# Optimization experiments

Measured on AMD Instinct MI355X. Metric: run time of the kernel, lower is better.

## Reference

```python
import jax, jax.numpy as jnp
import numpy as np

S = 4096   # decoder sequence length
T = 4096   # encoder sequence length
D = 2048   # x_size == qk_size (required for q @ k^T to typecheck)


def setup_inputs() -> dict:
    key = jax.random.key(0)
    k1, k2, k3, k4 = jax.random.split(key, 4)
    x_vectors = jax.random.normal(k1, (S, D), dtype=jnp.float32)
    enc_output = jax.random.normal(k2, (2, T, S), dtype=jnp.float32) * 0.02
    Wq = jax.random.normal(k3, (D, D), dtype=jnp.float32) * 0.02
    bq = jax.random.normal(k4, (D,), dtype=jnp.float32) * 0.02
    return {"x_vectors": x_vectors, "enc_output": enc_output, "Wq": Wq, "bq": bq}


def reference(x_vectors, enc_output, Wq, bq):
    # q = Linear(x): [S, D]
    q = x_vectors @ Wq.T + bq
    # k, v produced by matmul of encoder-output matrices with x: [T, D]
    k = enc_output[0] @ x_vectors
    v = enc_output[1] @ x_vectors
    # attention scores [S, T], scaled by sqrt(qk_size)
    e = (q @ k.T) / jnp.sqrt(jnp.float32(D))
    # softmax over dim=1 (last axis of the rank-2 score matrix)
    a = jax.nn.softmax(e, axis=1)
    # z = a @ v^T: [S, D]
    z = a @ v
    return z
```

## Files before the change

kernel.cpp:

```cpp
#include <hip/hip_runtime.h>


typedef __attribute__((ext_vector_type(8))) __bf16 bf16x8;
typedef __attribute__((ext_vector_type(4))) float f32x4;
typedef __attribute__((ext_vector_type(4))) unsigned short ushort4v;
typedef __attribute__((ext_vector_type(8))) unsigned short ushort8v;

#define S_DIM 4096
#define T_DIM 4096
#define D_DIM 2048

__device__ __forceinline__ unsigned short f2bf(float f) {
    unsigned int u = __float_as_uint(f);
    u += 0x7fffu + ((u >> 16) & 1u);
    return (unsigned short)(u >> 16);
}

__device__ __forceinline__ void block_sync() {
    __builtin_amdgcn_sched_barrier(0);
    __builtin_amdgcn_s_barrier();
    __builtin_amdgcn_sched_barrier(0);
}

#define GL(gptr, sptr)                                                        \
    __builtin_amdgcn_global_load_lds(                                         \
        (__attribute__((address_space(1))) void*)(void*)(gptr),               \
        (__attribute__((address_space(3))) void*)(sptr), 16, 0, 0)

__device__ __forceinline__ f32x4 MFMA(bf16x8 a, bf16x8 b, f32x4 c) {
    return __builtin_amdgcn_mfma_f32_16x16x32_bf16(a, b, c, 0, 0, 0);
}

__global__ __launch_bounds__(256)
void k_convert(const float* __restrict__ in, unsigned short* __restrict__ out, long n) {
    long i = ((long)blockIdx.x * blockDim.x + threadIdx.x) * 8;
    const long stride = (long)gridDim.x * blockDim.x * 8;
    for (; i < n; i += stride) {
        float4 a = *(const float4*)(in + i);
        float4 b = *(const float4*)(in + i + 4);
        ushort8v o;
        o[0] = f2bf(a.x); o[1] = f2bf(a.y); o[2] = f2bf(a.z); o[3] = f2bf(a.w);
        o[4] = f2bf(b.x); o[5] = f2bf(b.y); o[6] = f2bf(b.z); o[7] = f2bf(b.w);
        *(ushort8v*)(out + i) = o;
    }
}

__global__ __launch_bounds__(256)
void k_transpose(const float* __restrict__ in, unsigned short* __restrict__ out,
                 int R, int C) {
    __shared__ float tile[32][33];
    const int bx = blockIdx.x * 32;
    const int by = blockIdx.y * 32;
    const int tx = threadIdx.x;
    const int ty = threadIdx.y;
    #pragma unroll
    for (int i = 0; i < 32; i += 8)
        tile[ty + i][tx] = in[(long)(by + ty + i) * C + bx + tx];
    __syncthreads();
    #pragma unroll
    for (int i = 0; i < 32; i += 8)
        out[(long)(bx + ty + i) * R + by + tx] = f2bf(tile[tx][ty + i]);
}

__global__ __launch_bounds__(256)
void k_transpose_bf(const unsigned short* __restrict__ in,
                    unsigned short* __restrict__ out, int R, int C) {
    __shared__ unsigned short tile[32][33];
    const int bx = blockIdx.x * 32;
    const int by = blockIdx.y * 32;
    const int tx = threadIdx.x;
    const int ty = threadIdx.y;
    #pragma unroll
    for (int i = 0; i < 32; i += 8)
        tile[ty + i][tx] = in[(long)(by + ty + i) * C + bx + tx];
    __syncthreads();
    #pragma unroll
    for (int i = 0; i < 32; i += 8)
        out[(long)(bx + ty + i) * R + by + tx] = tile[tx][ty + i];
}

template<bool STG, bool PF, int VMW>
__device__ __forceinline__ void seg8(
    const unsigned short* (&gA)[2], const int (&ldA)[2],
    const unsigned short* (&gB)[2], const int (&ldB)[2],
    const char* cur, const char* nxt, char* stg, int arB, int brB,
    bf16x8 (&Ac)[8], bf16x8 (&B01c)[2], bf16x8 (&B23)[2],
    bf16x8 (&An)[8], bf16x8 (&B01n)[2],
    f32x4 (&acc)[8][4])
{
    B23[0] = *(const bf16x8*)(cur + brB + 2048);
    B23[1] = *(const bf16x8*)(cur + brB + 3072);
    if constexpr (STG) {
        GL(gA[0], stg + ldA[0]); gA[0] += 32;
        GL(gA[1], stg + ldA[1]); gA[1] += 32;
    }
    block_sync();
    asm volatile("s_waitcnt lgkmcnt(2)" ::: "memory");
    __builtin_amdgcn_sched_barrier(0);
    __builtin_amdgcn_s_setprio(1);
    #pragma unroll
    for (int m = 0; m < 8; ++m) {
        acc[m][0] = MFMA(Ac[m], B01c[0], acc[m][0]);
        acc[m][1] = MFMA(Ac[m], B01c[1], acc[m][1]);
    }
    __builtin_amdgcn_s_setprio(0);
    if constexpr (PF) {
        #pragma unroll
        for (int m = 0; m < 8; ++m)
            An[m] = *(const bf16x8*)(nxt + arB + m * 1024);
        B01n[0] = *(const bf16x8*)(nxt + brB);
        B01n[1] = *(const bf16x8*)(nxt + brB + 1024);
    }
    if constexpr (STG) {
        GL(gB[0], stg + ldB[0]); gB[0] += 32;
        GL(gB[1], stg + ldB[1]); gB[1] += 32;
    }
    if constexpr (VMW == 4)      asm volatile("s_waitcnt vmcnt(4)" ::: "memory");
    else if constexpr (VMW == 0) asm volatile("s_waitcnt vmcnt(0)" ::: "memory");
    block_sync();
    if constexpr (PF) asm volatile("s_waitcnt lgkmcnt(10)" ::: "memory");
    else              asm volatile("s_waitcnt lgkmcnt(0)" ::: "memory");
    __builtin_amdgcn_sched_barrier(0);
    __builtin_amdgcn_s_setprio(1);
    #pragma unroll
    for (int m = 0; m < 8; ++m) {
        acc[m][2] = MFMA(Ac[m], B23[0], acc[m][2]);
        acc[m][3] = MFMA(Ac[m], B23[1], acc[m][3]);
    }
    __builtin_amdgcn_s_setprio(0);
}

template<bool STG, bool PF, int VMW>
__device__ __forceinline__ void seg4(
    const unsigned short* (&gA)[2], const int (&ldA)[2],
    const unsigned short* (&gB)[2], const int (&ldB)[2],
    const char* nxt, char* stg, int arB, int brB,
    bf16x8 (&Ac)[4], bf16x8 (&Bc)[4],
    bf16x8 (&An)[4], bf16x8 (&Bn)[4],
    f32x4 (&acc)[4][4])
{
    if constexpr (PF) {
        #pragma unroll
        for (int m = 0; m < 4; ++m)
            An[m] = *(const bf16x8*)(nxt + arB + m * 1024);
        #pragma unroll
        for (int n = 0; n < 4; ++n)
            Bn[n] = *(const bf16x8*)(nxt + brB + n * 1024);
    }
    if constexpr (STG) {
        GL(gA[0], stg + ldA[0]); gA[0] += 32;
        GL(gB[0], stg + ldB[0]); gB[0] += 32;
        GL(gB[1], stg + ldB[1]); gB[1] += 32;
    }
    if constexpr (VMW == 3)      asm volatile("s_waitcnt vmcnt(3)" ::: "memory");
    else if constexpr (VMW == 0) asm volatile("s_waitcnt vmcnt(0)" ::: "memory");
    block_sync();
    if constexpr (PF) asm volatile("s_waitcnt lgkmcnt(8)" ::: "memory");
    else              asm volatile("s_waitcnt lgkmcnt(0)" ::: "memory");
    __builtin_amdgcn_sched_barrier(0);
    __builtin_amdgcn_s_setprio(1);
    #pragma unroll
    for (int m = 0; m < 4; ++m)
        #pragma unroll
        for (int n = 0; n < 4; ++n)
            acc[m][n] = MFMA(Ac[m], Bc[n], acc[m][n]);
    __builtin_amdgcn_s_setprio(0);
}

template<int MFR, int OUT_BF16, int HAS_BIAS>
__global__ __launch_bounds__(512, 2)
void k_gemm(const unsigned short* __restrict__ A,
            const unsigned short* __restrict__ B,
            const float* __restrict__ bias,
            void* __restrict__ C,
            int M, int N, int K, float alpha) {
    constexpr int BM   = MFR * 32;
    constexpr int LPTA = (BM * 4) / 512;
    constexpr int LDSA = BM * 64;
    constexpr int SLOT = LDSA + 16384;
    extern __shared__ __align__(16) char smem[];

    const int tid = threadIdx.x;
    const int l = tid & 63;
    const int w = tid >> 6;
    const int wr = w >> 2;
    const int wc = w & 3;

    const int gx = gridDim.x, gy = gridDim.y;
    const int flat = blockIdx.y * gx + blockIdx.x;
    const int per = (gx * gy) >> 3;
    const int wid = (flat & 7) * per + (flat >> 3);
    const int sc = wid / (gy * 4);
    const int rm = wid - sc * gy * 4;
    const int by = rm >> 2;
    const int bx = sc * 4 + (rm & 3);

    const long brow = (long)by * BM;
    const long bcol = (long)bx * 256;
    const int NT = K >> 5;

    const unsigned short* gA[2];
    int ldA[2];
    #pragma unroll
    for (int j = 0; j < LPTA; ++j) {
        const int q = (w * LPTA + j) * 64 + l;
        const int R = q >> 2;
        const int c = (q & 3) ^ ((R >> 1) & 3);
        gA[j] = A + (brow + R) * (long)K + c * 8;
        ldA[j] = q * 16;
    }
    const unsigned short* gB[2];
    int ldB[2];
    #pragma unroll
    for (int j = 0; j < 2; ++j) {
        const int q = (w * 2 + j) * 64 + l;
        const int R = q >> 2;
        const int c = (q & 3) ^ ((R >> 1) & 3);
        gB[j] = B + (bcol + R) * (long)K + c * 8;
        ldB[j] = LDSA + q * 16;
    }

    const int sAB = (((l >> 4) ^ ((l >> 1) & 3)) << 4);
    const int arB = (wr * (MFR * 16) + (l & 15)) * 64 + sAB;
    const int brB = LDSA + (wc * 64 + (l & 15)) * 64 + sAB;

    char* const b0 = smem;
    char* const b1 = smem + SLOT;
    char* const b2 = smem + 2 * SLOT;
    char* const b3 = smem + 3 * SLOT;

    f32x4 acc[MFR][4] = {};

    {
        char* d = smem;
        #pragma unroll
        for (int tt = 0; tt < 3; ++tt) {
            #pragma unroll
            for (int j = 0; j < LPTA; ++j) { GL(gA[j], d + ldA[j]); gA[j] += 32; }
            #pragma unroll
            for (int j = 0; j < 2; ++j)    { GL(gB[j], d + ldB[j]); gB[j] += 32; }
            d += SLOT;
        }
        if constexpr (MFR == 8) asm volatile("s_waitcnt vmcnt(4)" ::: "memory");
        else                    asm volatile("s_waitcnt vmcnt(3)" ::: "memory");
        block_sync();
    }

    if constexpr (MFR == 8) {
        bf16x8 Aa[8], Ab[8], Ba[2], Bb[2], B23[2];
        #pragma unroll
        for (int m = 0; m < 8; ++m) Aa[m] = *(const bf16x8*)(b0 + arB + m * 1024);
        Ba[0] = *(const bf16x8*)(b0 + brB);
        Ba[1] = *(const bf16x8*)(b0 + brB + 1024);

        for (int t = 0; t + 8 <= NT; t += 4) {
            seg8<true, true, 4>(gA, ldA, gB, ldB, b0, b1, b3, arB, brB,
                                Aa, Ba, B23, Ab, Bb, acc);
            seg8<true, true, 4>(gA, ldA, gB, ldB, b1, b2, b0, arB, brB,
                                Ab, Bb, B23, Aa, Ba, acc);
            seg8<true, true, 4>(gA, ldA, gB, ldB, b2, b3, b1, arB, brB,
                                Aa, Ba, B23, Ab, Bb, acc);
            seg8<true, true, 4>(gA, ldA, gB, ldB, b3, b0, b2, arB, brB,
                                Ab, Bb, B23, Aa, Ba, acc);
        }
        seg8<true,  true,  4>(gA, ldA, gB, ldB, b0, b1, b3, arB, brB,
                              Aa, Ba, B23, Ab, Bb, acc);
        seg8<false, true,  0>(gA, ldA, gB, ldB, b1, b2, b3, arB, brB,
                              Ab, Bb, B23, Aa, Ba, acc);
        seg8<false, true, -1>(gA, ldA, gB, ldB, b2, b3, b3, arB, brB,
                              Aa, Ba, B23, Ab, Bb, acc);
        seg8<false, false, -1>(gA, ldA, gB, ldB, b3, b0, b3, arB, brB,
                               Ab, Bb, B23, Aa, Ba, acc);
    } else {
        bf16x8 Aa[4], Ab[4], Ba[4], Bb[4];
        #pragma unroll
        for (int m = 0; m < 4; ++m) Aa[m] = *(const bf16x8*)(b0 + arB + m * 1024);
        #pragma unroll
        for (int n = 0; n < 4; ++n) Ba[n] = *(const bf16x8*)(b0 + brB + n * 1024);

        for (int t = 0; t + 8 <= NT; t += 4) {
            seg4<true, true, 3>(gA, ldA, gB, ldB, b1, b3, arB, brB, Aa, Ba, Ab, Bb, acc);
            seg4<true, true, 3>(gA, ldA, gB, ldB, b2, b0, arB, brB, Ab, Bb, Aa, Ba, acc);
            seg4<true, true, 3>(gA, ldA, gB, ldB, b3, b1, arB, brB, Aa, Ba, Ab, Bb, acc);
            seg4<true, true, 3>(gA, ldA, gB, ldB, b0, b2, arB, brB, Ab, Bb, Aa, Ba, acc);
        }
        seg4<true,  true,  3>(gA, ldA, gB, ldB, b1, b3, arB, brB, Aa, Ba, Ab, Bb, acc);
        seg4<false, true,  0>(gA, ldA, gB, ldB, b2, b3, arB, brB, Ab, Bb, Aa, Ba, acc);
        seg4<false, true, -1>(gA, ldA, gB, ldB, b3, b3, arB, brB, Aa, Ba, Ab, Bb, acc);
        seg4<false, false, -1>(gA, ldA, gB, ldB, b3, b3, arB, brB, Ab, Bb, Aa, Ba, acc);
    }

    const long crow0 = brow + wr * (MFR * 16) + (l >> 4) * 4;
    const long ccol0 = bcol + wc * 64 + (l & 15);
    #pragma unroll
    for (int n = 0; n < 4; ++n) {
        const long col = ccol0 + n * 16;
        const float bb = HAS_BIAS ? bias[col] : 0.0f;
        #pragma unroll
        for (int m = 0; m < MFR; ++m) {
            #pragma unroll
            for (int r = 0; r < 4; ++r) {
                const long row = crow0 + m * 16 + r;
                const float v = acc[m][n][r] * alpha + bb;
                if (OUT_BF16)
                    ((unsigned short*)C)[row * N + col] = f2bf(v);
                else
                    ((float*)C)[row * N + col] = v;
            }
        }
    }
}

__global__ __launch_bounds__(256)
void k_softmax(const float* __restrict__ E, unsigned short* __restrict__ A, int T) {
    const long row = blockIdx.x;
    const float* er = E + row * (long)T;
    const int t = threadIdx.x;
    const int l = t & 63;
    const int w = t >> 6;

    float4 v[4];
    float m = -3.4e38f;
    #pragma unroll
    for (int j = 0; j < 4; ++j) {
        v[j] = *(const float4*)(er + j * 1024 + t * 4);
        m = fmaxf(m, fmaxf(fmaxf(v[j].x, v[j].y), fmaxf(v[j].z, v[j].w)));
    }
    #pragma unroll
    for (int o = 32; o > 0; o >>= 1) m = fmaxf(m, __shfl_xor(m, o));

    __shared__ float redm[4];
    __shared__ float reds[4];
    if (l == 0) redm[w] = m;
    __syncthreads();
    m = fmaxf(fmaxf(redm[0], redm[1]), fmaxf(redm[2], redm[3]));

    float s = 0.f;
    #pragma unroll
    for (int j = 0; j < 4; ++j) {
        v[j].x = __expf(v[j].x - m); s += v[j].x;
        v[j].y = __expf(v[j].y - m); s += v[j].y;
        v[j].z = __expf(v[j].z - m); s += v[j].z;
        v[j].w = __expf(v[j].w - m); s += v[j].w;
    }
    #pragma unroll
    for (int o = 32; o > 0; o >>= 1) s += __shfl_xor(s, o);
    if (l == 0) reds[w] = s;
    __syncthreads();
    s = reds[0] + reds[1] + reds[2] + reds[3];
    const float inv = 1.0f / s;

    unsigned short* ar = A + row * (long)T;
    #pragma unroll
    for (int j = 0; j < 4; ++j) {
        ushort4v o4;
        o4[0] = f2bf(v[j].x * inv);
        o4[1] = f2bf(v[j].y * inv);
        o4[2] = f2bf(v[j].z * inv);
        o4[3] = f2bf(v[j].w * inv);
        *(ushort4v*)(ar + j * 1024 + t * 4) = o4;
    }
}

extern "C" void kernel_launch(void* const* d_in, const int* in_sizes, int n_in,
                              void* d_out, int out_size, void* d_ws, size_t ws_size,
                              hipStream_t stream) {
    const float* x   = (const float*)d_in[0];
    const float* enc = (const float*)d_in[1];
    const float* Wq  = (const float*)d_in[2];
    const float* bq  = (const float*)d_in[3];
    float* out = (float*)d_out;
    char* ws = (char*)d_ws;

    unsigned short* abf   = (unsigned short*)(ws);
    unsigned short* xT    = (unsigned short*)(ws);
    unsigned short* xbf   = (unsigned short*)(ws + (16L << 20));
    unsigned short* wqbf  = (unsigned short*)(ws + (32L << 20));
    unsigned short* qbf   = (unsigned short*)(ws + (40L << 20));
    unsigned short* kv    = (unsigned short*)(ws + (56L << 20));
    unsigned short* vT    = (unsigned short*)(ws + (88L << 20));
    unsigned short* encbf = (unsigned short*)(ws + (104L << 20));
    float*          e     = (float*)(ws + (104L << 20));

    k_convert<<<4096, 256, 0, stream>>>(x,   xbf,   (long)S_DIM * D_DIM);
    k_convert<<<4096, 256, 0, stream>>>(Wq,  wqbf,  (long)D_DIM * D_DIM);
    k_convert<<<4096, 256, 0, stream>>>(enc, encbf, 2L * T_DIM * S_DIM);
    k_transpose<<<dim3(D_DIM / 32, S_DIM / 32), dim3(32, 8), 0, stream>>>(x, xT, S_DIM, D_DIM);

    #define LAUNCH_G(MFRV, OB, HB, Ap, Bp, biasp, Cp, M_, N_, K_, al)                      \
        do {                                                                               \
            constexpr int smemB = (MFRV * 32 * 64 + 16384) * 4;                            \
            hipFuncSetAttribute((const void*)k_gemm<MFRV, OB, HB>,                         \
                                hipFuncAttributeMaxDynamicSharedMemorySize, smemB);        \
            k_gemm<MFRV, OB, HB><<<dim3((N_) / 256, (M_) / (MFRV * 32)), 512, smemB,       \
                                   stream>>>(Ap, Bp, biasp, Cp, M_, N_, K_, al);           \
        } while (0)

    LAUNCH_G(4, 1, 1, xbf, wqbf, bq, qbf, S_DIM, D_DIM, D_DIM, 1.0f);
    LAUNCH_G(8, 1, 0, encbf, xT, nullptr, kv, 2 * T_DIM, D_DIM, S_DIM, 1.0f);
    k_transpose_bf<<<dim3(D_DIM / 32, T_DIM / 32), dim3(32, 8), 0, stream>>>(
        kv + (long)T_DIM * D_DIM, vT, T_DIM, D_DIM);
    LAUNCH_G(8, 0, 0, qbf, kv, nullptr, e, S_DIM, T_DIM, D_DIM, 0.022097086912079608f);
    k_softmax<<<S_DIM, 256, 0, stream>>>(e, abf, T_DIM);
    LAUNCH_G(4, 0, 0, abf, vT, nullptr, out, S_DIM, D_DIM, T_DIM, 1.0f);
}
```

Before: 377.1 us.

## Use 32x32x16 MFMA in large-tile GEMM and fuse x conversion into transpose

The MFR=8 GEMM path switches from 16x16x32 to 32x32x16 bf16 MFMA instructions, reworking LDS read addressing (XOR-swizzled halves), accumulator layout and the epilogue row mapping. Larger MFMA tiles cut instruction count and fragment reuse overhead. Separately, the x-to-bf16 conversion kernel is merged into the transpose kernel, which now writes both layouts from one read of x. The risk is higher register pressure and a less coalesced epilogue store pattern.

```diff
diff --git a/kernel.cpp b/kernel.cpp
--- a/kernel.cpp
+++ b/kernel.cpp
@@ -3,6 +3,7 @@
 
 typedef __attribute__((ext_vector_type(8))) __bf16 bf16x8;
 typedef __attribute__((ext_vector_type(4))) float f32x4;
+typedef __attribute__((ext_vector_type(16))) float f32x16;
 typedef __attribute__((ext_vector_type(4))) unsigned short ushort4v;
 typedef __attribute__((ext_vector_type(8))) unsigned short ushort8v;
 
@@ -27,8 +28,11 @@
         (__attribute__((address_space(1))) void*)(void*)(gptr),               \
         (__attribute__((address_space(3))) void*)(sptr), 16, 0, 0)
 
-__device__ __forceinline__ f32x4 MFMA(bf16x8 a, bf16x8 b, f32x4 c) {
+__device__ __forceinline__ f32x4 MFMA16(bf16x8 a, bf16x8 b, f32x4 c) {
     return __builtin_amdgcn_mfma_f32_16x16x32_bf16(a, b, c, 0, 0, 0);
+}
+__device__ __forceinline__ f32x16 MFMA32(bf16x8 a, bf16x8 b, f32x16 c) {
+    return __builtin_amdgcn_mfma_f32_32x32x16_bf16(a, b, c, 0, 0, 0);
 }
 
 __global__ __launch_bounds__(256)
@@ -46,20 +50,24 @@
 }
 
 __global__ __launch_bounds__(256)
-void k_transpose(const float* __restrict__ in, unsigned short* __restrict__ out,
-                 int R, int C) {
+void k_transpose_dual(const float* __restrict__ in,
+                      unsigned short* __restrict__ outT,
+                      unsigned short* __restrict__ outN, int R, int C) {
     __shared__ float tile[32][33];
     const int bx = blockIdx.x * 32;
     const int by = blockIdx.y * 32;
     const int tx = threadIdx.x;
     const int ty = threadIdx.y;
     #pragma unroll
+    for (int i = 0; i < 32; i += 8) {
+        float v = in[(long)(by + ty + i) * C + bx + tx];
+        tile[ty + i][tx] = v;
+        outN[(long)(by + ty + i) * C + bx + tx] = f2bf(v);
+    }
+    __syncthreads();
+    #pragma unroll
     for (int i = 0; i < 32; i += 8)
-        tile[ty + i][tx] = in[(long)(by + ty + i) * C + bx + tx];
-    __syncthreads();
-    #pragma unroll
-    for (int i = 0; i < 32; i += 8)
-        out[(long)(bx + ty + i) * R + by + tx] = f2bf(tile[tx][ty + i]);
+        outT[(long)(bx + ty + i) * R + by + tx] = f2bf(tile[tx][ty + i]);
 }
 
 __global__ __launch_bounds__(256)
@@ -80,16 +88,16 @@
 }
 
 template<bool STG, bool PF, int VMW>
-__device__ __forceinline__ void seg8(
+__device__ __forceinline__ void seg32(
     const unsigned short* (&gA)[2], const int (&ldA)[2],
     const unsigned short* (&gB)[2], const int (&ldB)[2],
     const char* cur, const char* nxt, char* stg, int arB, int brB,
-    bf16x8 (&Ac)[8], bf16x8 (&B01c)[2], bf16x8 (&B23)[2],
-    bf16x8 (&An)[8], bf16x8 (&B01n)[2],
-    f32x4 (&acc)[8][4])
+    bf16x8 (&Ac)[8], bf16x8 (&B0c)[2], bf16x8 (&B1)[2],
+    bf16x8 (&An)[8], bf16x8 (&B0n)[2],
+    f32x16 (&acc)[4][2])
 {
-    B23[0] = *(const bf16x8*)(cur + brB + 2048);
-    B23[1] = *(const bf16x8*)(cur + brB + 3072);
+    B1[0] = *(const bf16x8*)(cur + (brB + 2048));
+    B1[1] = *(const bf16x8*)(cur + ((brB + 2048) ^ 32));
     if constexpr (STG) {
         GL(gA[0], stg + ldA[0]); gA[0] += 32;
         GL(gA[1], stg + ldA[1]); gA[1] += 32;
@@ -99,17 +107,19 @@
     __builtin_amdgcn_sched_barrier(0);
     __builtin_amdgcn_s_setprio(1);
     #pragma unroll
-    for (int m = 0; m < 8; ++m) {
-        acc[m][0] = MFMA(Ac[m], B01c[0], acc[m][0]);
-        acc[m][1] = MFMA(Ac[m], B01c[1], acc[m][1]);
+    for (int mt = 0; mt < 4; ++mt) {
+        acc[mt][0] = MFMA32(Ac[mt * 2 + 0], B0c[0], acc[mt][0]);
+        acc[mt][0] = MFMA32(Ac[mt * 2 + 1], B0c[1], acc[mt][0]);
     }
     __builtin_amdgcn_s_setprio(0);
     if constexpr (PF) {
         #pragma unroll
-        for (int m = 0; m < 8; ++m)
-            An[m] = *(const bf16x8*)(nxt + arB + m * 1024);
-        B01n[0] = *(const bf16x8*)(nxt + brB);
-        B01n[1] = *(const bf16x8*)(nxt + brB + 1024);
+        for (int mt = 0; mt < 4; ++mt) {
+            An[mt * 2 + 0] = *(const bf16x8*)(nxt + (arB + mt * 2048));
+            An[mt * 2 + 1] = *(const bf16x8*)(nxt + ((arB + mt * 2048) ^ 32));
+        }
+        B0n[0] = *(const bf16x8*)(nxt + brB);
+        B0n[1] = *(const bf16x8*)(nxt + (brB ^ 32));
     }
     if constexpr (STG) {
         GL(gB[0], stg + ldB[0]); gB[0] += 32;
@@ -123,9 +133,9 @@
     __builtin_amdgcn_sched_barrier(0);
     __builtin_amdgcn_s_setprio(1);
     #pragma unroll
-    for (int m = 0; m < 8; ++m) {
-        acc[m][2] = MFMA(Ac[m], B23[0], acc[m][2]);
-        acc[m][3] = MFMA(Ac[m], B23[1], acc[m][3]);
+    for (int mt = 0; mt < 4; ++mt) {
+        acc[mt][1] = MFMA32(Ac[mt * 2 + 0], B1[0], acc[mt][1]);
+        acc[mt][1] = MFMA32(Ac[mt * 2 + 1], B1[1], acc[mt][1]);
     }
     __builtin_amdgcn_s_setprio(0);
 }
@@ -163,7 +173,7 @@
     for (int m = 0; m < 4; ++m)
         #pragma unroll
         for (int n = 0; n < 4; ++n)
-            acc[m][n] = MFMA(Ac[m], Bc[n], acc[m][n]);
+            acc[m][n] = MFMA16(Ac[m], Bc[n], acc[m][n]);
     __builtin_amdgcn_s_setprio(0);
 }
 
@@ -220,16 +230,10 @@
         ldB[j] = LDSA + q * 16;
     }
 
-    const int sAB = (((l >> 4) ^ ((l >> 1) & 3)) << 4);
-    const int arB = (wr * (MFR * 16) + (l & 15)) * 64 + sAB;
-    const int brB = LDSA + (wc * 64 + (l & 15)) * 64 + sAB;
-
     char* const b0 = smem;
     char* const b1 = smem + SLOT;
     char* const b2 = smem + 2 * SLOT;
     char* const b3 = smem + 3 * SLOT;
-
-    f32x4 acc[MFR][4] = {};
 
     {
         char* d = smem;
@@ -247,31 +251,65 @@
     }
 
     if constexpr (MFR == 8) {
-        bf16x8 Aa[8], Ab[8], Ba[2], Bb[2], B23[2];
-        #pragma unroll
-        for (int m = 0; m < 8; ++m) Aa[m] = *(const bf16x8*)(b0 + arB + m * 1024);
-        Ba[0] = *(const bf16x8*)(b0 + brB);
-        Ba[1] = *(const bf16x8*)(b0 + brB + 1024);
+        const int hi = l >> 5;
+        const int sw = (l >> 1) & 3;
+        const int s0 = ((hi ^ sw) << 4);
+        const int arB = (wr * 128 + (l & 31)) * 64 + s0;
+        const int brB = LDSA + (wc * 64 + (l & 31)) * 64 + s0;
+
+        f32x16 acc[4][2] = {};
+        bf16x8 Aa[8], Ab[8], B0a[2], B0b[2], B1[2];
+        #pragma unroll
+        for (int mt = 0; mt < 4; ++mt) {
+            Aa[mt * 2 + 0] = *(const bf16x8*)(b0 + (arB + mt * 2048));
+            Aa[mt * 2 + 1] = *(const bf16x8*)(b0 + ((arB + mt * 2048) ^ 32));
+        }
+        B0a[0] = *(const bf16x8*)(b0 + brB);
+        B0a[1] = *(const bf16x8*)(b0 + (brB ^ 32));
 
         for (int t = 0; t + 8 <= NT; t += 4) {
-            seg8<true, true, 4>(gA, ldA, gB, ldB, b0, b1, b3, arB, brB,
-                                Aa, Ba, B23, Ab, Bb, acc);
-            seg8<true, true, 4>(gA, ldA, gB, ldB, b1, b2, b0, arB, brB,
-                                Ab, Bb, B23, Aa, Ba, acc);
-            seg8<true, true, 4>(gA, ldA, gB, ldB, b2, b3, b1, arB, brB,
-                                Aa, Ba, B23, Ab, Bb, acc);
-            seg8<true, true, 4>(gA, ldA, gB, ldB, b3, b0, b2, arB, brB,
-                                Ab, Bb, B23, Aa, Ba, acc);
-        }
-        seg8<true,  true,  4>(gA, ldA, gB, ldB, b0, b1, b3, arB, brB,
-                              Aa, Ba, B23, Ab, Bb, acc);
-        seg8<false, true,  0>(gA, ldA, gB, ldB, b1, b2, b3, arB, brB,
-                              Ab, Bb, B23, Aa, Ba, acc);
-        seg8<false, true, -1>(gA, ldA, gB, ldB, b2, b3, b3, arB, brB,
-                              Aa, Ba, B23, Ab, Bb, acc);
-        seg8<false, false, -1>(gA, ldA, gB, ldB, b3, b0, b3, arB, brB,
-                               Ab, Bb, B23, Aa, Ba, acc);
+            seg32<true, true, 4>(gA, ldA, gB, ldB, b0, b1, b3, arB, brB,
+                                 Aa, B0a, B1, Ab, B0b, acc);
+            seg32<true, true, 4>(gA, ldA, gB, ldB, b1, b2, b0, arB, brB,
+                                 Ab, B0b, B1, Aa, B0a, acc);
+            seg32<true, true, 4>(gA, ldA, gB, ldB, b2, b3, b1, arB, brB,
+                                 Aa, B0a, B1, Ab, B0b, acc);
+            seg32<true, true, 4>(gA, ldA, gB, ldB, b3, b0, b2, arB, brB,
+                                 Ab, B0b, B1, Aa, B0a, acc);
+        }
+        seg32<true,  true,  4>(gA, ldA, gB, ldB, b0, b1, b3, arB, brB,
+                               Aa, B0a, B1, Ab, B0b, acc);
+        seg32<false, true,  0>(gA, ldA, gB, ldB, b1, b2, b3, arB, brB,
+                               Ab, B0b, B1, Aa, B0a, acc);
+        seg32<false, true, -1>(gA, ldA, gB, ldB, b2, b3, b3, arB, brB,
+                               Aa, B0a, B1, Ab, B0b, acc);
+        seg32<false, false, -1>(gA, ldA, gB, ldB, b3, b0, b3, arB, brB,
+                                Ab, B0b, B1, Aa, B0a, acc);
+
+        #pragma unroll
+        for (int nt = 0; nt < 2; ++nt) {
+            const long col = bcol + wc * 64 + nt * 32 + (l & 31);
+            const float bb = HAS_BIAS ? bias[col] : 0.0f;
+            #pragma unroll
+            for (int mt = 0; mt < 4; ++mt) {
+                #pragma unroll
+                for (int reg = 0; reg < 16; ++reg) {
+                    const long row = brow + wr * 128 + mt * 32 +
+                                     (reg & 3) + 8 * (reg >> 2) + 4 * hi;
+                    const float v = acc[mt][nt][reg] * alpha + bb;
+                    if (OUT_BF16)
+                        ((unsigned short*)C)[row * N + col] = f2bf(v);
+                    else
+                        ((float*)C)[row * N + col] = v;
+                }
+            }
+        }
     } else {
+        const int sAB = (((l >> 4) ^ ((l >> 1) & 3)) << 4);
+        const int arB = (wr * (MFR * 16) + (l & 15)) * 64 + sAB;
+        const int brB = LDSA + (wc * 64 + (l & 15)) * 64 + sAB;
+
+        f32x4 acc[4][4] = {};
         bf16x8 Aa[4], Ab[4], Ba[4], Bb[4];
         #pragma unroll
         for (int m = 0; m < 4; ++m) Aa[m] = *(const bf16x8*)(b0 + arB + m * 1024);
@@ -288,24 +326,24 @@
         seg4<false, true,  0>(gA, ldA, gB, ldB, b2, b3, arB, brB, Ab, Bb, Aa, Ba, acc);
         seg4<false, true, -1>(gA, ldA, gB, ldB, b3, b3, arB, brB, Aa, Ba, Ab, Bb, acc);
         seg4<false, false, -1>(gA, ldA, gB, ldB, b3, b3, arB, brB, Ab, Bb, Aa, Ba, acc);
-    }
-
-    const long crow0 = brow + wr * (MFR * 16) + (l >> 4) * 4;
-    const long ccol0 = bcol + wc * 64 + (l & 15);
-    #pragma unroll
-    for (int n = 0; n < 4; ++n) {
-        const long col = ccol0 + n * 16;
-        const float bb = HAS_BIAS ? bias[col] : 0.0f;
-        #pragma unroll
-        for (int m = 0; m < MFR; ++m) {
+
+        const long crow0 = brow + wr * (MFR * 16) + (l >> 4) * 4;
+        const long ccol0 = bcol + wc * 64 + (l & 15);
+        #pragma unroll
+        for (int n = 0; n < 4; ++n) {
+            const long col = ccol0 + n * 16;
+            const float bb = HAS_BIAS ? bias[col] : 0.0f;
             #pragma unroll
-            for (int r = 0; r < 4; ++r) {
-                const long row = crow0 + m * 16 + r;
-                const float v = acc[m][n][r] * alpha + bb;
-                if (OUT_BF16)
-                    ((unsigned short*)C)[row * N + col] = f2bf(v);
-                else
-                    ((float*)C)[row * N + col] = v;
+            for (int m = 0; m < 4; ++m) {
+                #pragma unroll
+                for (int r = 0; r < 4; ++r) {
+                    const long row = crow0 + m * 16 + r;
+                    const float v = acc[m][n][r] * alpha + bb;
+                    if (OUT_BF16)
+                        ((unsigned short*)C)[row * N + col] = f2bf(v);
+                    else
+                        ((float*)C)[row * N + col] = v;
+                }
             }
         }
     }
@@ -382,10 +420,10 @@
     unsigned short* encbf = (unsigned short*)(ws + (104L << 20));
     float*          e     = (float*)(ws + (104L << 20));
 
-    k_convert<<<4096, 256, 0, stream>>>(x,   xbf,   (long)S_DIM * D_DIM);
     k_convert<<<4096, 256, 0, stream>>>(Wq,  wqbf,  (long)D_DIM * D_DIM);
     k_convert<<<4096, 256, 0, stream>>>(enc, encbf, 2L * T_DIM * S_DIM);
-    k_transpose<<<dim3(D_DIM / 32, S_DIM / 32), dim3(32, 8), 0, stream>>>(x, xT, S_DIM, D_DIM);
+    k_transpose_dual<<<dim3(D_DIM / 32, S_DIM / 32), dim3(32, 8), 0, stream>>>(
+        x, xT, xbf, S_DIM, D_DIM);
 
     #define LAUNCH_G(MFRV, OB, HB, Ap, Bp, biasp, Cp, M_, N_, K_, al)                      \
         do {                                                                               \
```

Result: slower. 417.1 us (+10.6%).
